# Kernel optimization log

Measured on AMD Instinct MI355X. Metric: run time of the kernel, lower is better.

Reference implementation:

```python
import jax, jax.numpy as jnp
import numpy as np
from math import factorial

# ---------- real-basis Wigner 3j (Clebsch-Gordan) constants ----------

def _su2_cg(j1, j2, j3, m1, m2, m3):
    if m3 != m1 + m2 or not (abs(j1 - j2) <= j3 <= j1 + j2):
        return 0.0
    f = factorial
    pref = ((2 * j3 + 1) * f(j3 + j1 - j2) * f(j3 - j1 + j2) * f(j1 + j2 - j3) / f(j1 + j2 + j3 + 1)) ** 0.5
    pref *= (f(j3 + m3) * f(j3 - m3) * f(j1 - m1) * f(j1 + m1) * f(j2 - m2) * f(j2 + m2)) ** 0.5
    s = 0.0
    for k in range(0, j1 + j2 - j3 + 1):
        args = [k, j1 + j2 - j3 - k, j1 - m1 - k, j2 + m2 - k, j3 - j2 + m1 + k, j3 - j1 - m2 + k]
        if any(a < 0 for a in args):
            continue
        d = 1.0
        for a in args:
            d *= f(a)
        s += (-1) ** k / d
    return pref * s


def _q(l):  # complex->real spherical harmonics change of basis (e3nn convention)
    q = np.zeros((2 * l + 1, 2 * l + 1), dtype=complex)
    for m in range(-l, 0):
        q[l + m, l + abs(m)] = 2 ** -0.5
        q[l + m, l - abs(m)] = -1j * 2 ** -0.5
    q[l, l] = 1.0
    for m in range(1, l + 1):
        q[l + m, l + abs(m)] = (-1) ** m * 2 ** -0.5
        q[l + m, l - abs(m)] = 1j * (-1) ** m * 2 ** -0.5
    return (-1j) ** l * q


def _wigner3j(l1, l2, l3):
    C = np.zeros((2 * l1 + 1, 2 * l2 + 1, 2 * l3 + 1))
    for m1 in range(-l1, l1 + 1):
        for m2 in range(-l2, l2 + 1):
            m3 = m1 + m2
            if -l3 <= m3 <= l3:
                C[l1 + m1, l2 + m2, l3 + m3] = _su2_cg(l1, l2, l3, m1, m2, m3)
    T = np.einsum('ai,bj,ck,ijk->abc', _q(l1), _q(l2), np.conj(_q(l3)), C)
    T = T.real if np.abs(T.real).sum() >= np.abs(T.imag).sum() else T.imag
    return (T / (2 * l3 + 1) ** 0.5).astype(np.float32)  # 3j normalization


LS = [0, 1, 2]                       # Rs_mid irreps (each multiplicity 1)
OFF = {0: (0, 1), 1: (1, 4), 2: (4, 9)}  # slices into the dim-9 irrep vector
L_OUT = [0, 1, 2, 3, 4]
MUL_OUT = {0: 64, 1: 64, 2: 64, 3: 32, 4: 16}
MUL_MID = 32
CG = {(l1, l2, l3): jnp.asarray(_wigner3j(l1, l2, l3))
      for l1 in LS for l2 in LS for l3 in range(abs(l1 - l2), l1 + l2 + 1)}


def setup_inputs():
    key = jax.random.key(0)
    ks = jax.random.split(key, 8)
    N = 50000
    x1 = jax.random.normal(ks[0], (N, MUL_MID * 9), jnp.float32)
    x2 = jax.random.normal(ks[1], (N, MUL_MID * 9), jnp.float32)
    n_paths = {l: 0 for l in L_OUT}
    for (_, _, l3) in CG:
        n_paths[l3] += 1
    out = {"x1": x1, "x2": x2}
    for i, l in enumerate(L_OUT):
        out[f"W{l}"] = jax.random.normal(ks[2 + i], (MUL_OUT[l], n_paths[l] * MUL_MID), jnp.float32)
    return out


def _forward(x1, x2, Ws):
    n = x1.shape[0]
    a = x1.reshape(n, MUL_MID, 9)
    b = x2.reshape(n, MUL_MID, 9)
    blocks = {l: [] for l in L_OUT}
    for l1 in LS:
        s1 = a[:, :, OFF[l1][0]:OFF[l1][1]]
        for l2 in LS:
            s2 = b[:, :, OFF[l2][0]:OFF[l2][1]]
            for l3 in range(abs(l1 - l2), l1 + l2 + 1):
                # [n, mul, 2l3+1] CG-gated bilinear contraction per channel
                blocks[l3].append(jnp.einsum('nui,nuj,ijk->nuk', s1, s2, CG[(l1, l2, l3)]))
    outs = []
    for l in L_OUT:
        feat = jnp.concatenate(blocks[l], axis=1)        # [n, mul_in, 2l+1]
        mul_in = feat.shape[1]
        o = jnp.einsum('nui,ou->noi', feat, Ws[l] / np.float32(np.sqrt(mul_in)))
        outs.append(o.reshape(n, -1))
    return jnp.concatenate(outs, axis=1)                 # [n, 944]


def reference(x1, x2, W0, W1, W2, W3, W4):
    return _forward(x1, x2, {0: W0, 1: W1, 2: W2, 3: W3, 4: W4})
```

## Files before the change

### kernel.cpp

```cpp
#include <hip/hip_runtime.h>
#include <hip/hip_fp16.h>
#include <array>

typedef __attribute__((ext_vector_type(8))) _Float16 f16x8;
typedef __attribute__((ext_vector_type(4))) float f32x4;
typedef __attribute__((ext_vector_type(4))) unsigned u32x4;

#define N_PATHS 19
#define SROW 148
#define SROWH 298

constexpr int kPL1[N_PATHS]  = {0,0,0,1,1,1,1,1,1,1,2,2,2,2,2,2,2,2,2};
constexpr int kPL2[N_PATHS]  = {0,1,2,0,1,1,1,2,2,2,0,1,1,1,2,2,2,2,2};
constexpr int kPL3[N_PATHS]  = {0,1,2,1,0,1,2,1,2,3,2,1,2,3,0,1,2,3,4};
constexpr int kIOFF[3]  = {0,1,4};
constexpr int kSP[5][6] = {{0,4,14,0,0,0},{1,3,5,7,11,15},{2,6,8,10,12,16},{9,13,17,0,0,0},{18,0,0,0,0,0}};
constexpr int kKS[5] = {3,6,6,3,1};
constexpr int kNT[5] = {4,4,4,2,1};
constexpr int kOB[5] = {0,64,256,576,800};
constexpr int kFB[5] = {0,12,36,60,66};
#define N_FRAGS 67

struct ccplx { double re, im; };
constexpr ccplx cmulc(ccplx a, ccplx b){ return {a.re*b.re - a.im*b.im, a.re*b.im + a.im*b.re}; }
constexpr double cfact(int n){ double f = 1.0; for (int i = 2; i <= n; ++i) f *= i; return f; }
constexpr double csqrt(double x){
  if (x <= 0.0) return 0.0;
  double g = x > 1.0 ? x : 1.0;
  for (int i = 0; i < 64; ++i) g = 0.5*(g + x/g);
  return g;
}
constexpr double c_su2cg(int j1,int j2,int j3,int m1,int m2){
  int m3 = m1+m2;
  int am3 = m3 < 0 ? -m3 : m3;
  int dj = j1-j2 < 0 ? j2-j1 : j1-j2;
  if (j3 < dj || j3 > j1+j2 || am3 > j3) return 0.0;
  double pref = (2.0*j3+1.0)*cfact(j3+j1-j2)*cfact(j3-j1+j2)*cfact(j1+j2-j3)/cfact(j1+j2+j3+1);
  pref = csqrt(pref);
  pref *= csqrt(cfact(j3+m3)*cfact(j3-m3)*cfact(j1-m1)*cfact(j1+m1)*cfact(j2-m2)*cfact(j2+m2));
  double s = 0.0;
  for (int k = 0; k <= j1+j2-j3; ++k){
    int a1=j1+j2-j3-k, a2=j1-m1-k, a3=j2+m2-k, a4=j3-j2+m1+k, a5=j3-j1-m2+k;
    if (a1<0||a2<0||a3<0||a4<0||a5<0) continue;
    double d = cfact(k)*cfact(a1)*cfact(a2)*cfact(a3)*cfact(a4)*cfact(a5);
    s += ((k&1) ? -1.0 : 1.0)/d;
  }
  return pref*s;
}
constexpr ccplx qel(int l, int r, int c){
  const double rt = 0.70710678118654752440;
  int m = r - l;
  ccplx v{0.0, 0.0};
  if (m < 0){
    if (c == l - m) v = {rt, 0.0};
    else if (c == l + m) v = {0.0, -rt};
  } else if (m == 0){
    if (c == l) v = {1.0, 0.0};
  } else {
    double s = (m & 1) ? -1.0 : 1.0;
    if (c == l + m) v = {s*rt, 0.0};
    else if (c == l - m) v = {0.0, s*rt};
  }
  int ph = l & 3;
  if (ph == 1) return { v.im, -v.re};
  if (ph == 2) return {-v.re, -v.im};
  if (ph == 3) return {-v.im,  v.re};
  return v;
}
template<int P>
constexpr auto make_cg(){
  constexpr int l1 = kPL1[P], l2 = kPL2[P], l3 = kPL3[P];
  constexpr int D1 = 2*l1+1, D2v = 2*l2+1, D3 = 2*l3+1;
  double su[D1][D2v] = {};
  for (int i = 0; i < D1; ++i)
    for (int j = 0; j < D2v; ++j)
      su[i][j] = c_su2cg(l1, l2, l3, i-l1, j-l2);
  std::array<double, (size_t)D1*D2v*D3> re{}, im{};
  double sre = 0.0, sim = 0.0;
  for (int a = 0; a < D1; ++a)
    for (int b = 0; b < D2v; ++b)
      for (int c = 0; c < D3; ++c){
        ccplx acc{0.0, 0.0};
        for (int i = 0; i < D1; ++i)
          for (int j = 0; j < D2v; ++j){
            int kk = l3 + (i-l1) + (j-l2);
            if (kk < 0 || kk >= D3) continue;
            double cgv = su[i][j];
            if (cgv == 0.0) continue;
            ccplx q3 = qel(l3, c, kk);
            ccplx pr = cmulc(cmulc(qel(l1,a,i), qel(l2,b,j)), ccplx{q3.re, -q3.im});
            acc.re += pr.re*cgv; acc.im += pr.im*cgv;
          }
        size_t e = ((size_t)a*D2v + b)*D3 + c;
        re[e] = acc.re; im[e] = acc.im;
        sre += acc.re < 0 ? -acc.re : acc.re;
        sim += acc.im < 0 ? -acc.im : acc.im;
      }
  std::array<float, (size_t)D1*D2v*D3> out{};
  const bool useRe = (sre >= sim);
  const double norm = 1.0/csqrt((double)D3);
  for (size_t e = 0; e < out.size(); ++e){
    double v = (useRe ? re[e] : im[e])*norm;
    if (v < 1e-10 && v > -1e-10) v = 0.0;
    out[e] = (float)v;
  }
  return out;
}
template<int P> struct CGTab { static constexpr auto tab = make_cg<P>(); };
template<int P, int K> constexpr bool row_any(int E){
  for (int k = 0; k < K; ++k) if (CGTab<P>::tab[(size_t)E*K + k] != 0.0f) return true;
  return false;
}
constexpr unsigned short h_bits(double v){
  if (v == 0.0) return 0;
  unsigned short s = 0;
  if (v < 0){ s = 0x8000; v = -v; }
  int e = 0;
  while (v >= 2.0){ v *= 0.5; ++e; }
  while (v < 1.0){ v *= 2.0; --e; }
  double m = (v - 1.0) * 1024.0;
  int mi = (int)(m + 0.5);
  if (mi == 1024){ mi = 0; ++e; }
  return (unsigned short)(s | ((unsigned)(e + 15) << 10) | (unsigned)mi);
}
constexpr unsigned h2_bits(double v){
  unsigned short h = h_bits(v);
  return (unsigned)h | ((unsigned)h << 16);
}

__global__ void prep_w_kernel(const float* __restrict__ W0, const float* __restrict__ W1,
                              const float* __restrict__ W2, const float* __restrict__ W3,
                              const float* __restrict__ W4, unsigned short* __restrict__ wout){
  int el = blockIdx.x*256 + threadIdx.x;
  if (el >= N_FRAGS*512) return;
  int frag = el>>9, r = el&511, lam = r>>3, j = r&7;
  int l  = (frag<12)?0 : (frag<36)?1 : (frag<60)?2 : (frag<66)?3 : 4;
  int fb = (l==0)?0 : (l==1)?12 : (l==2)?36 : (l==3)?60 : 66;
  int Ks = (l==0)?3 : (l==1)?6 : (l==2)?6 : (l==3)?3 : 1;
  int U  = (l==0)?96 : (l==1)?192 : (l==2)?192 : (l==3)?96 : 32;
  int rel = frag - fb, nt = rel/Ks, tt = rel - nt*Ks;
  int o = nt*16 + (lam&15);
  int u = tt*32 + (lam>>4)*8 + j;
  const float* W = (l==0)?W0 : (l==1)?W1 : (l==2)?W2 : (l==3)?W3 : W4;
  float scale = (l==0||l==3) ? 0.10206207261596575f
              : (l==4)       ? 0.17677669529663687f
                             : 0.07216878364870323f;
  wout[el] = __half_as_ushort(__float2half_rn(W[o*U + u] * scale));
}


template<int P, int K, int E, int KK>
struct PKk {
  static __device__ __forceinline__ void run(__half2 (&a)[K], __half2 p){
    constexpr float w = CGTab<P>::tab[(size_t)E*K + KK];
    if constexpr (w != 0.0f){
      constexpr unsigned W2 = h2_bits((double)w);
      a[KK] = __hfma2(__builtin_bit_cast(__half2, W2), p, a[KK]);
    }
    if constexpr (KK+1 < K) PKk<P,K,E,KK+1>::run(a, p);
  }
};

template<int P, int K, int D2v, int E, int NE>
struct PElem {
  static __device__ __forceinline__ void run(__half2 (&a)[K],
                                             const __half2* xa, const __half2* xb){
    if constexpr (row_any<P,K>(E)){
      constexpr int i = E / D2v, jj = E - i*D2v;
      __half2 p = __hmul2(xa[i], xb[jj]);
      PKk<P,K,E,0>::run(a, p);
    }
    if constexpr (E+1 < NE) PElem<P,K,D2v,E+1,NE>::run(a, xa, xb);
  }
};

template<int L, int TT>
struct TTF {
  static constexpr int P  = kSP[L][TT];
  static constexpr int L1 = kPL1[P], L2_ = kPL2[P];
  static constexpr int D1 = 2*L1+1, D2v = 2*L2_+1;
  static constexpr int O1 = kIOFF[L1], O2 = kIOFF[L2_];
  static constexpr int K = 2*L+1, Ks = kKS[L], Nt = kNT[L];
  static __device__ __forceinline__ void run(f32x4 (&acc)[kNT[L]][2*L+1],
                                             const __half* i1p, const __half* i2p,
                                             const short* wf){
    u32x4 af[K];
    #pragma unroll
    for (int jp=0; jp<4; ++jp){
      __half2 xa[D1], xb[D2v];
      #pragma unroll
      for (int i=0;i<D1;++i)
        xa[i] = *reinterpret_cast<const __half2*>(i1p + (O1+i)*8 + jp*2);
      #pragma unroll
      for (int j=0;j<D2v;++j)
        xb[j] = *reinterpret_cast<const __half2*>(i2p + (O2+j)*8 + jp*2);
      __half2 a[K];
      #pragma unroll
      for (int k=0;k<K;++k) a[k] = __builtin_bit_cast(__half2, 0u);
      PElem<P,K,D2v,0,D1*D2v>::run(a, xa, xb);
      #pragma unroll
      for (int k=0;k<K;++k) af[k][jp] = __builtin_bit_cast(unsigned, a[k]);
    }
    #pragma unroll
    for (int nt=0; nt<Nt; ++nt){
      const f16x8 bf = *reinterpret_cast<const f16x8*>(wf + (nt*Ks+TT)*512);
      #pragma unroll
      for (int k=0;k<K;++k)
        acc[nt][k] = __builtin_amdgcn_mfma_f32_16x16x32_f16(
                       __builtin_bit_cast(f16x8, af[k]), bf, acc[nt][k], 0, 0, 0);
    }
    if constexpr (TT+1 < Ks) TTF<L,TT+1>::run(acc, i1p, i2p, wf);
  }
};

template<int L>
__device__ __forceinline__ void do_group(const __half* __restrict__ i1p,
                                         const __half* __restrict__ i2p,
                                         const short* __restrict__ wfrag,
                                         float* slab, float* __restrict__ out,
                                         int nrowb, int N, int lane){
  constexpr int K = 2*L+1, Nt = kNT[L];
  const int s = lane&15, g = lane>>4;
  f32x4 acc[Nt][K];
  #pragma unroll
  for (int nt=0;nt<Nt;++nt)
    #pragma unroll
    for (int k=0;k<K;++k) acc[nt][k] = (f32x4){0.f,0.f,0.f,0.f};

  const short* wf = wfrag + (size_t)kFB[L]*512 + (size_t)lane*8;
  TTF<L,0>::run(acc, i1p, i2p, wf);

  #pragma unroll
  for (int nt=0; nt<Nt; ++nt){
    #pragma unroll
    for (int k=0;k<K;++k)
      #pragma unroll
      for (int r=0;r<4;++r)
        slab[(g*4+r)*SROW + s*K + k] = acc[nt][k][r];
    const int rr = lane>>2, q4 = lane&3;
    const float* sp = slab + rr*SROW;
    const bool on = (nrowb + rr) < N;
    float* op = out + (size_t)(nrowb+rr)*944 + kOB[L] + nt*16*K;
    #pragma unroll
    for (int c=0;c<K;++c){
      float4 v = *reinterpret_cast<const float4*>(sp + (c*4+q4)*4);
      if (on) *reinterpret_cast<float4*>(op + (c*4+q4)*4) = v;
    }
  }
}

__global__ __launch_bounds__(128, 2) void tp_main(
    const float* __restrict__ x1, const float* __restrict__ x2,
    const short* __restrict__ wfrag, float* __restrict__ out, int N)
{
  __shared__ __align__(16) __half in1h[16*SROWH];
  __shared__ __align__(16) __half in2h[16*SROWH];
  __shared__ __align__(16) float stage[2*16*SROW];
  const int t = threadIdx.x, w = t>>6, lane = t&63;
  const int nb = blockIdx.x*16;

  for (int idx = t; idx < 16*72; idx += 128){
    int row = idx/72, c4 = idx - row*72;
    int n = nb + row;
    float4 v1 = {0,0,0,0}, v2 = {0,0,0,0};
    if (n < N){
      v1 = reinterpret_cast<const float4*>(x1 + (size_t)n*288)[c4];
      v2 = reinterpret_cast<const float4*>(x2 + (size_t)n*288)[c4];
    }
    float a1v[4] = {v1.x, v1.y, v1.z, v1.w};
    float a2v[4] = {v2.x, v2.y, v2.z, v2.w};
    #pragma unroll
    for (int u=0; u<4; ++u){
      int c = c4*4 + u;
      int m = c/9, e = c - m*9;
      int g = m>>3, j = m&7;
      int haddr = row*SROWH + g*72 + e*8 + j;
      in1h[haddr] = __float2half_rn(a1v[u]);
      in2h[haddr] = __float2half_rn(a2v[u]);
    }
  }
  __syncthreads();

  const int s = lane&15, g = lane>>4;
  const __half* i1p = &in1h[s*SROWH + g*72];
  const __half* i2p = &in2h[s*SROWH + g*72];
  float* slab = &stage[w*16*SROW];

  if (w == 0){
    do_group<0>(i1p, i2p, wfrag, slab, out, nb, N, lane);
    do_group<1>(i1p, i2p, wfrag, slab, out, nb, N, lane);
    do_group<3>(i1p, i2p, wfrag, slab, out, nb, N, lane);
  } else {
    do_group<2>(i1p, i2p, wfrag, slab, out, nb, N, lane);
    do_group<4>(i1p, i2p, wfrag, slab, out, nb, N, lane);
  }
}

extern "C" void kernel_launch(void* const* d_in, const int* in_sizes, int n_in,
                              void* d_out, int out_size, void* d_ws, size_t ws_size,
                              hipStream_t stream)
{
  (void)n_in; (void)out_size; (void)ws_size;
  const float* x1 = (const float*)d_in[0];
  const float* x2 = (const float*)d_in[1];
  const float* W0 = (const float*)d_in[2];
  const float* W1 = (const float*)d_in[3];
  const float* W2 = (const float*)d_in[4];
  const float* W3 = (const float*)d_in[5];
  const float* W4 = (const float*)d_in[6];
  float* out = (float*)d_out;
  int N = in_sizes[0] / 288;

  prep_w_kernel<<<dim3((N_FRAGS*512 + 255)/256), dim3(256), 0, stream>>>(
      W0, W1, W2, W3, W4, (unsigned short*)d_ws);
  int grid = (N + 15) / 16;
  tp_main<<<dim3(grid), dim3(128), 0, stream>>>(
      x1, x2, (const short*)d_ws, out, N);
}
```

Before: 89.31 us.

## Split output groups across four waves and stage results in fp16 shared memory

```diff
diff --git a/kernel.cpp b/kernel.cpp
--- a/kernel.cpp
+++ b/kernel.cpp
@@ -7,7 +7,6 @@
 typedef __attribute__((ext_vector_type(4))) unsigned u32x4;
 
 #define N_PATHS 19
-#define SROW 148
 #define SROWH 298
 
 constexpr int kPL1[N_PATHS]  = {0,0,0,1,1,1,1,1,1,1,2,2,2,2,2,2,2,2,2};
@@ -128,6 +127,8 @@
   return (unsigned)h | ((unsigned)h << 16);
 }
 
+__device__ __forceinline__ void cfence(){ asm volatile("" ::: "memory"); }
+
 __global__ void prep_w_kernel(const float* __restrict__ W0, const float* __restrict__ W1,
                               const float* __restrict__ W2, const float* __restrict__ W3,
                               const float* __restrict__ W4, unsigned short* __restrict__ wout){
@@ -174,14 +175,14 @@
   }
 };
 
-template<int L, int TT>
+template<int L, int TT, int NTB, int NTE>
 struct TTF {
   static constexpr int P  = kSP[L][TT];
   static constexpr int L1 = kPL1[P], L2_ = kPL2[P];
   static constexpr int D1 = 2*L1+1, D2v = 2*L2_+1;
   static constexpr int O1 = kIOFF[L1], O2 = kIOFF[L2_];
-  static constexpr int K = 2*L+1, Ks = kKS[L], Nt = kNT[L];
-  static __device__ __forceinline__ void run(f32x4 (&acc)[kNT[L]][2*L+1],
+  static constexpr int K = 2*L+1, Ks = kKS[L];
+  static __device__ __forceinline__ void run(f32x4 (&acc)[NTE-NTB][2*L+1],
                                              const __half* i1p, const __half* i2p,
                                              const short* wf){
     u32x4 af[K];
@@ -202,64 +203,73 @@
       for (int k=0;k<K;++k) af[k][jp] = __builtin_bit_cast(unsigned, a[k]);
     }
     #pragma unroll
-    for (int nt=0; nt<Nt; ++nt){
+    for (int nt=NTB; nt<NTE; ++nt){
       const f16x8 bf = *reinterpret_cast<const f16x8*>(wf + (nt*Ks+TT)*512);
       #pragma unroll
       for (int k=0;k<K;++k)
-        acc[nt][k] = __builtin_amdgcn_mfma_f32_16x16x32_f16(
-                       __builtin_bit_cast(f16x8, af[k]), bf, acc[nt][k], 0, 0, 0);
-    }
-    if constexpr (TT+1 < Ks) TTF<L,TT+1>::run(acc, i1p, i2p, wf);
+        acc[nt-NTB][k] = __builtin_amdgcn_mfma_f32_16x16x32_f16(
+                           __builtin_bit_cast(f16x8, af[k]), bf, acc[nt-NTB][k], 0, 0, 0);
+    }
+    if constexpr (TT+1 < Ks) TTF<L,TT+1,NTB,NTE>::run(acc, i1p, i2p, wf);
   }
 };
 
 template<int L>
-__device__ __forceinline__ void do_group(const __half* __restrict__ i1p,
-                                         const __half* __restrict__ i2p,
-                                         const short* __restrict__ wfrag,
-                                         float* slab, float* __restrict__ out,
-                                         int nrowb, int N, int lane){
-  constexpr int K = 2*L+1, Nt = kNT[L];
+__device__ __forceinline__ void do_flush(const __half* slabh, float* __restrict__ out,
+                                         int nrowb, int N, int lane, int nt){
+  constexpr int K = 2*L+1, SH = 16*K+8;
+  cfence();
+  #pragma unroll
+  for (int c=0;c<K;++c){
+    int idx = lane + 64*c;
+    int row = idx/(4*K), j = idx - row*(4*K);
+    __half2 h0 = *reinterpret_cast<const __half2*>(slabh + row*SH + j*4);
+    __half2 h1 = *reinterpret_cast<const __half2*>(slabh + row*SH + j*4 + 2);
+    float4 v = {__low2float(h0), __high2float(h0), __low2float(h1), __high2float(h1)};
+    if (nrowb + row < N)
+      *reinterpret_cast<float4*>(out + (size_t)(nrowb+row)*944 + kOB[L] + nt*16*K + j*4) = v;
+  }
+  cfence();
+}
+
+template<int L, int NTB, int NTE>
+__device__ __forceinline__ void group_unit(const __half* i1p, const __half* i2p,
+                                           const short* __restrict__ wfrag,
+                                           __half* slabh, float* __restrict__ out,
+                                           int nrowb, int N, int lane){
+  constexpr int K = 2*L+1, SH = 16*K+8;
   const int s = lane&15, g = lane>>4;
-  f32x4 acc[Nt][K];
+  f32x4 acc[NTE-NTB][K];
   #pragma unroll
-  for (int nt=0;nt<Nt;++nt)
-    #pragma unroll
-    for (int k=0;k<K;++k) acc[nt][k] = (f32x4){0.f,0.f,0.f,0.f};
+  for (int a=0;a<NTE-NTB;++a)
+    #pragma unroll
+    for (int k=0;k<K;++k) acc[a][k] = (f32x4){0.f,0.f,0.f,0.f};
 
   const short* wf = wfrag + (size_t)kFB[L]*512 + (size_t)lane*8;
-  TTF<L,0>::run(acc, i1p, i2p, wf);
+  TTF<L,0,NTB,NTE>::run(acc, i1p, i2p, wf);
 
   #pragma unroll
-  for (int nt=0; nt<Nt; ++nt){
+  for (int nt=NTB; nt<NTE; ++nt){
     #pragma unroll
     for (int k=0;k<K;++k)
       #pragma unroll
       for (int r=0;r<4;++r)
-        slab[(g*4+r)*SROW + s*K + k] = acc[nt][k][r];
-    const int rr = lane>>2, q4 = lane&3;
-    const float* sp = slab + rr*SROW;
-    const bool on = (nrowb + rr) < N;
-    float* op = out + (size_t)(nrowb+rr)*944 + kOB[L] + nt*16*K;
-    #pragma unroll
-    for (int c=0;c<K;++c){
-      float4 v = *reinterpret_cast<const float4*>(sp + (c*4+q4)*4);
-      if (on) *reinterpret_cast<float4*>(op + (c*4+q4)*4) = v;
-    }
-  }
-}
-
-__global__ __launch_bounds__(128, 2) void tp_main(
+        slabh[(g*4+r)*SH + s*K + k] = __float2half_rn(acc[nt-NTB][k][r]);
+    do_flush<L>(slabh, out, nrowb, N, lane, nt);
+  }
+}
+
+__global__ __launch_bounds__(256, 4) void tp_main(
     const float* __restrict__ x1, const float* __restrict__ x2,
     const short* __restrict__ wfrag, float* __restrict__ out, int N)
 {
   __shared__ __align__(16) __half in1h[16*SROWH];
   __shared__ __align__(16) __half in2h[16*SROWH];
-  __shared__ __align__(16) float stage[2*16*SROW];
+  __shared__ __align__(16) __half slab[6144];
   const int t = threadIdx.x, w = t>>6, lane = t&63;
   const int nb = blockIdx.x*16;
 
-  for (int idx = t; idx < 16*72; idx += 128){
+  for (int idx = t; idx < 16*72; idx += 256){
     int row = idx/72, c4 = idx - row*72;
     int n = nb + row;
     float4 v1 = {0,0,0,0}, v2 = {0,0,0,0};
@@ -273,8 +283,8 @@
     for (int u=0; u<4; ++u){
       int c = c4*4 + u;
       int m = c/9, e = c - m*9;
-      int g = m>>3, j = m&7;
-      int haddr = row*SROWH + g*72 + e*8 + j;
+      int gg = m>>3, j = m&7;
+      int haddr = row*SROWH + gg*72 + e*8 + j;
       in1h[haddr] = __float2half_rn(a1v[u]);
       in2h[haddr] = __float2half_rn(a2v[u]);
     }
@@ -284,15 +294,18 @@
   const int s = lane&15, g = lane>>4;
   const __half* i1p = &in1h[s*SROWH + g*72];
   const __half* i2p = &in2h[s*SROWH + g*72];
-  float* slab = &stage[w*16*SROW];
+  __half* slabh = slab + (w==0 ? 0 : w==1 ? 896 : w==2 ? 2304 : 3712);
 
   if (w == 0){
-    do_group<0>(i1p, i2p, wfrag, slab, out, nb, N, lane);
-    do_group<1>(i1p, i2p, wfrag, slab, out, nb, N, lane);
-    do_group<3>(i1p, i2p, wfrag, slab, out, nb, N, lane);
+    group_unit<1,0,4>(i1p, i2p, wfrag, slabh, out, nb, N, lane);
+  } else if (w == 1){
+    group_unit<2,0,2>(i1p, i2p, wfrag, slabh, out, nb, N, lane);
+  } else if (w == 2){
+    group_unit<2,2,4>(i1p, i2p, wfrag, slabh, out, nb, N, lane);
+    group_unit<0,0,4>(i1p, i2p, wfrag, slabh, out, nb, N, lane);
   } else {
-    do_group<2>(i1p, i2p, wfrag, slab, out, nb, N, lane);
-    do_group<4>(i1p, i2p, wfrag, slab, out, nb, N, lane);
+    group_unit<3,0,2>(i1p, i2p, wfrag, slabh, out, nb, N, lane);
+    group_unit<4,0,1>(i1p, i2p, wfrag, slabh, out, nb, N, lane);
   }
 }
 
@@ -314,6 +327,6 @@
   prep_w_kernel<<<dim3((N_FRAGS*512 + 255)/256), dim3(256), 0, stream>>>(
       W0, W1, W2, W3, W4, (unsigned short*)d_ws);
   int grid = (N + 15) / 16;
-  tp_main<<<dim3(grid), dim3(128), 0, stream>>>(
+  tp_main<<<dim3(grid), dim3(256), 0, stream>>>(
       x1, x2, (const short*)d_ws, out, N);
 }
```

Result: slower. 114.5 us (+28.2%).

## Split output groups across three waves and stage results in fp16 LDS

Applied to the files above, without the earlier changes.

```diff
diff --git a/kernel.cpp b/kernel.cpp
--- a/kernel.cpp
+++ b/kernel.cpp
@@ -7,7 +7,6 @@
 typedef __attribute__((ext_vector_type(4))) unsigned u32x4;
 
 #define N_PATHS 19
-#define SROW 148
 #define SROWH 298
 
 constexpr int kPL1[N_PATHS]  = {0,0,0,1,1,1,1,1,1,1,2,2,2,2,2,2,2,2,2};
@@ -128,6 +127,8 @@
   return (unsigned)h | ((unsigned)h << 16);
 }
 
+__device__ __forceinline__ void cfence(){ asm volatile("" ::: "memory"); }
+
 __global__ void prep_w_kernel(const float* __restrict__ W0, const float* __restrict__ W1,
                               const float* __restrict__ W2, const float* __restrict__ W3,
                               const float* __restrict__ W4, unsigned short* __restrict__ wout){
@@ -214,12 +215,30 @@
 };
 
 template<int L>
+__device__ __forceinline__ void do_flush(const __half* slabh, float* __restrict__ out,
+                                         int nrowb, int N, int lane, int nt){
+  constexpr int K = 2*L+1, SH = 16*K+8;
+  cfence();
+  #pragma unroll
+  for (int c=0;c<K;++c){
+    int idx = lane + 64*c;
+    int row = idx/(4*K), j = idx - row*(4*K);
+    __half2 h0 = *reinterpret_cast<const __half2*>(slabh + row*SH + j*4);
+    __half2 h1 = *reinterpret_cast<const __half2*>(slabh + row*SH + j*4 + 2);
+    float4 v = {__low2float(h0), __high2float(h0), __low2float(h1), __high2float(h1)};
+    if (nrowb + row < N)
+      *reinterpret_cast<float4*>(out + (size_t)(nrowb+row)*944 + kOB[L] + nt*16*K + j*4) = v;
+  }
+  cfence();
+}
+
+template<int L>
 __device__ __forceinline__ void do_group(const __half* __restrict__ i1p,
                                          const __half* __restrict__ i2p,
                                          const short* __restrict__ wfrag,
-                                         float* slab, float* __restrict__ out,
+                                         __half* slabh, float* __restrict__ out,
                                          int nrowb, int N, int lane){
-  constexpr int K = 2*L+1, Nt = kNT[L];
+  constexpr int K = 2*L+1, Nt = kNT[L], SH = 16*K+8;
   const int s = lane&15, g = lane>>4;
   f32x4 acc[Nt][K];
   #pragma unroll
@@ -236,30 +255,22 @@
     for (int k=0;k<K;++k)
       #pragma unroll
       for (int r=0;r<4;++r)
-        slab[(g*4+r)*SROW + s*K + k] = acc[nt][k][r];
-    const int rr = lane>>2, q4 = lane&3;
-    const float* sp = slab + rr*SROW;
-    const bool on = (nrowb + rr) < N;
-    float* op = out + (size_t)(nrowb+rr)*944 + kOB[L] + nt*16*K;
-    #pragma unroll
-    for (int c=0;c<K;++c){
-      float4 v = *reinterpret_cast<const float4*>(sp + (c*4+q4)*4);
-      if (on) *reinterpret_cast<float4*>(op + (c*4+q4)*4) = v;
-    }
-  }
-}
-
-__global__ __launch_bounds__(128, 2) void tp_main(
+        slabh[(g*4+r)*SH + s*K + k] = __float2half_rn(acc[nt][k][r]);
+    do_flush<L>(slabh, out, nrowb, N, lane, nt);
+  }
+}
+
+__global__ __launch_bounds__(192, 4) void tp_main(
     const float* __restrict__ x1, const float* __restrict__ x2,
     const short* __restrict__ wfrag, float* __restrict__ out, int N)
 {
   __shared__ __align__(16) __half in1h[16*SROWH];
   __shared__ __align__(16) __half in2h[16*SROWH];
-  __shared__ __align__(16) float stage[2*16*SROW];
+  __shared__ __align__(16) __half slab[5760];
   const int t = threadIdx.x, w = t>>6, lane = t&63;
   const int nb = blockIdx.x*16;
 
-  for (int idx = t; idx < 16*72; idx += 128){
+  for (int idx = t; idx < 16*72; idx += 192){
     int row = idx/72, c4 = idx - row*72;
     int n = nb + row;
     float4 v1 = {0,0,0,0}, v2 = {0,0,0,0};
@@ -273,8 +284,8 @@
     for (int u=0; u<4; ++u){
       int c = c4*4 + u;
       int m = c/9, e = c - m*9;
-      int g = m>>3, j = m&7;
-      int haddr = row*SROWH + g*72 + e*8 + j;
+      int gg = m>>3, j = m&7;
+      int haddr = row*SROWH + gg*72 + e*8 + j;
       in1h[haddr] = __float2half_rn(a1v[u]);
       in2h[haddr] = __float2half_rn(a2v[u]);
     }
@@ -284,15 +295,17 @@
   const int s = lane&15, g = lane>>4;
   const __half* i1p = &in1h[s*SROWH + g*72];
   const __half* i2p = &in2h[s*SROWH + g*72];
-  float* slab = &stage[w*16*SROW];
+  __half* slabh = slab + (w==0 ? 0 : w==1 ? 2432 : 3840);
 
   if (w == 0){
-    do_group<0>(i1p, i2p, wfrag, slab, out, nb, N, lane);
-    do_group<1>(i1p, i2p, wfrag, slab, out, nb, N, lane);
-    do_group<3>(i1p, i2p, wfrag, slab, out, nb, N, lane);
+    group: ;
+    do_group<1>(i1p, i2p, wfrag, slabh, out, nb, N, lane);
+    do_group<4>(i1p, i2p, wfrag, slabh, out, nb, N, lane);
+  } else if (w == 1){
+    do_group<2>(i1p, i2p, wfrag, slabh, out, nb, N, lane);
   } else {
-    do_group<2>(i1p, i2p, wfrag, slab, out, nb, N, lane);
-    do_group<4>(i1p, i2p, wfrag, slab, out, nb, N, lane);
+    do_group<3>(i1p, i2p, wfrag, slabh, out, nb, N, lane);
+    do_group<0>(i1p, i2p, wfrag, slabh, out, nb, N, lane);
   }
 }
 
@@ -314,6 +327,6 @@
   prep_w_kernel<<<dim3((N_FRAGS*512 + 255)/256), dim3(256), 0, stream>>>(
       W0, W1, W2, W3, W4, (unsigned short*)d_ws);
   int grid = (N + 15) / 16;
-  tp_main<<<dim3(grid), dim3(128), 0, stream>>>(
+  tp_main<<<dim3(grid), dim3(192), 0, stream>>>(
       x1, x2, (const short*)d_ws, out, N);
 }
```

Result: slower. 160.9 us (+80.1%).
